# Optimization experiments

Measured on AMD Instinct MI355X. Metric: run time of the kernel, lower is better.

The kernel has to match this reference:

```python
import jax, jax.numpy as jnp
import numpy as np

B, T, HID = 1, 2048, 1024
H, D = 16, 64
S = 64            # selection_block_size / sliding window / compress block
MAXK = 8          # max_selected_blocks
W_ENT, W_SP = 0.01, 0.01
NB = T // S       # 32 blocks (T divisible by S -> no padding branch)


def setup_inputs() -> dict:
    key = jax.random.key(0)
    ks = jax.random.split(key, 8)
    rn = lambda k, shp, s=0.02: jax.random.normal(k, shp, jnp.float32) * s
    return {
        'hidden_states': rn(ks[0], (B, T, HID), 1.0),
        'Wq': rn(ks[1], (HID, H * D)),
        'Wk': rn(ks[2], (HID, H * D)),
        'Wv': rn(ks[3], (HID, H * D)),
        'Wo': rn(ks[4], (H * D, HID)),
        'Wc': rn(ks[5], (S * D, D)),      # shared k/v compress MLP (same module in torch)
        'bc': jnp.zeros((D,), jnp.float32),
        'k_scale': jnp.ones((1,), jnp.float32),
        'k_bias': jnp.zeros((1,), jnp.float32),
        'Ws': rn(ks[6], (HID, 3 * H)),
        'bs': jnp.zeros((3 * H,), jnp.float32),
    }


def _local_attn(q, k, v):
    # lucidrains LocalAttention: window S, causal, look_backward=1, scale d^-0.5
    b, h, t, d = q.shape
    nw = t // S
    qw = q.reshape(b, h, nw, S, d)
    kw = k.reshape(b, h, nw, S, d)
    vw = v.reshape(b, h, nw, S, d)
    k_prev = jnp.concatenate([jnp.zeros_like(kw[:, :, :1]), kw[:, :, :-1]], axis=2)
    v_prev = jnp.concatenate([jnp.zeros_like(vw[:, :, :1]), vw[:, :, :-1]], axis=2)
    kc = jnp.concatenate([k_prev, kw], axis=3)   # (b,h,nw,2S,d)
    vc = jnp.concatenate([v_prev, vw], axis=3)
    scores = jnp.einsum('bhwid,bhwjd->bhwij', qw, kc) / jnp.sqrt(jnp.float32(d))
    qpos = jnp.arange(S)[:, None]
    krel = jnp.arange(2 * S)[None, :] - S        # key pos relative to window start
    wins = jnp.arange(nw)[:, None, None]
    allowed = (krel <= qpos)[None] & (wins * S + krel[None] >= 0)  # (nw,S,2S)
    NEG = -jnp.finfo(scores.dtype).max
    scores = jnp.where(allowed[None, None], scores, NEG)
    p = jax.nn.softmax(scores, axis=-1)
    return jnp.einsum('bhwij,bhwjd->bhwid', p, vc).reshape(b, h, t, d)


def reference(hidden_states, Wq, Wk, Wv, Wo, Wc, bc, k_scale, k_bias, Ws, bs):
    x = hidden_states
    scale = 1.0 / jnp.sqrt(jnp.float32(D))
    q = (x @ Wq).reshape(B, T, H, D).transpose(0, 2, 1, 3)
    k = (x @ Wk).reshape(B, T, H, D).transpose(0, 2, 1, 3)
    v = (x @ Wv).reshape(B, T, H, D).transpose(0, 2, 1, 3)

    sliding_out = _local_attn(q, k, v)

    # block compression (shared MLP for k and v, exact-erf GELU as in torch)
    k_blk = k.reshape(B, H, NB, S * D)
    v_blk = v.reshape(B, H, NB, S * D)
    kc = jax.nn.gelu(k_blk @ Wc + bc, approximate=False)   # (B,H,NB,D)
    vc = jax.nn.gelu(v_blk @ Wc + bc, approximate=False)

    importance = jnp.einsum('bhid,bhjd->bhij', q, kc) * scale   # (B,H,T,NB)
    comp_probs = jax.nn.softmax(importance, axis=-1)
    comp_out = jnp.einsum('bhij,bhjd->bhid', comp_probs, vc)

    # per-query-block scores, entropy-driven dynamic k
    block_scores = importance.reshape(B, H, NB, S, NB).mean(axis=3)   # (B,H,NB,NB)
    block_probs = jax.nn.softmax(block_scores, axis=-1)
    entropy = -jnp.sum(block_probs * jnp.log(block_probs + 1e-9), axis=-1)
    max_entropy = jnp.log(jnp.float32(NB))
    norm_ent = entropy / (max_entropy + 1e-9)
    k_ratio = jax.nn.sigmoid(k_scale[0] * norm_ent + k_bias[0])
    dynamic_k = jnp.clip(MAXK * k_ratio, 1.0, float(MAXK)).astype(jnp.int32)  # torch .long() truncates
    avg_k = dynamic_k.astype(jnp.float32).mean()

    _, topk_idx = jax.lax.top_k(block_scores, MAXK)                 # (B,H,NB,MAXK)
    k_mask = jnp.arange(MAXK)[None, None, None, :] < dynamic_k[..., None]
    sel = (topk_idx[..., None] == jnp.arange(NB)) & k_mask[..., None]
    mask = sel.any(axis=-2)                                         # (B,H,NB,NB)
    mask = mask | jnp.eye(NB, dtype=bool)[None, None]
    sparse_mask = jnp.repeat(jnp.repeat(mask, S, axis=2), S, axis=3)  # (B,H,T,T)

    attn = jnp.einsum('bhid,bhjd->bhij', q, k) * scale
    NEG = -jnp.finfo(attn.dtype).max
    attn = jnp.where(sparse_mask, attn, NEG)
    fine_probs = jax.nn.softmax(attn, axis=-1)
    fine_out = jnp.einsum('bhij,bhjd->bhid', fine_probs, v)

    strategy = jax.nn.sigmoid(x @ Ws + bs).reshape(B, T, H, 3).transpose(0, 2, 1, 3)  # (B,H,T,3)
    combined = jnp.stack([sliding_out, comp_out, fine_out], axis=-1)  # (B,H,T,D,3)
    out = jnp.einsum('bhnds,bhns->bhnd', combined, strategy)
    merged = out.transpose(0, 2, 1, 3).reshape(B, T, H * D)
    output = merged @ Wo

    entropy_loss = jnp.mean((k_ratio - norm_ent) ** 2)
    aux_loss = W_ENT * entropy_loss + W_SP * k_ratio.mean()
    return output, avg_k, aux_loss
```

## Files before the change

### kernel.cpp

```cpp
#include <hip/hip_runtime.h>
#include <math.h>
#include <stdint.h>

typedef unsigned short u16;
typedef short v8s __attribute__((ext_vector_type(8)));
typedef float v4f __attribute__((ext_vector_type(4)));

constexpr int kT   = 2048;
constexpr int kHID = 1024;
constexpr int kH   = 16;
constexpr int kNB  = 32;
constexpr size_t MB = 1ull << 20;

__device__ __forceinline__ float b2f(u16 u) { unsigned x = ((unsigned)u) << 16; return __uint_as_float(x); }
__device__ __forceinline__ u16 f2b(float f) {
  unsigned x = __float_as_uint(f);
  x += 0x7FFFu + ((x >> 16) & 1u);
  return (u16)(x >> 16);
}
__device__ __forceinline__ v4f mfma16(v8s a, v8s b, v4f c) {
  return __builtin_amdgcn_mfma_f32_16x16x32_bf16(a, b, c, 0, 0, 0);
}
__device__ __forceinline__ void gl_lds16(const void* g, void* l) {
  __builtin_amdgcn_global_load_lds((const __attribute__((address_space(1))) uint32_t*)g,
                                   (__attribute__((address_space(3))) uint32_t*)l, 16, 0, 0);
}

__global__ __launch_bounds__(256) void prep_kernel(
    const float* __restrict__ x, const float* __restrict__ Wq, const float* __restrict__ Wk,
    const float* __restrict__ Wv, const float* __restrict__ Wo, const float* __restrict__ Wc,
    const float* __restrict__ Wsp,
    u16* __restrict__ xh,
    u16* __restrict__ WqtH, u16* __restrict__ WktH,
    u16* __restrict__ WvtH, u16* __restrict__ WotH, u16* __restrict__ WctH, u16* __restrict__ WctL,
    u16* __restrict__ Wst) {
  __shared__ float tbuf[32][33];
  int bid = blockIdx.x;
  const int tid = threadIdx.x;
  if (bid < 1024) {
    int i = bid * 2048 + tid * 8;
    float4 a = *(const float4*)(x + i), b = *(const float4*)(x + i + 4);
    float tv[8] = {a.x, a.y, a.z, a.w, b.x, b.y, b.z, b.w};
    union { u16 s[8]; uint4 u; } hs;
#pragma unroll
    for (int e = 0; e < 8; ++e) hs.s[e] = f2b(tv[e]);
    *(uint4*)(xh + i) = hs.u;
    return;
  }
  bid -= 1024;
  const float* W; u16* Hh; u16* Ll; int Kd, Nd, bx, by;
  if (bid < 4096) {
    int wsel = bid >> 10, sub = bid & 1023;
    W  = wsel == 0 ? Wq : wsel == 1 ? Wk : wsel == 2 ? Wv : Wo;
    Hh = wsel == 0 ? WqtH : wsel == 1 ? WktH : wsel == 2 ? WvtH : WotH;
    Ll = nullptr;
    Kd = 1024; Nd = 1024;
    bx = (sub & 31) * 32; by = (sub >> 5) * 32;
  } else if (bid < 4096 + 256) {
    int sub = bid - 4096;
    W = Wc; Hh = WctH; Ll = WctL;
    Kd = 4096; Nd = 64;
    bx = (sub & 1) * 32; by = (sub >> 1) * 32;
  } else {
    int i = (bid - 4096 - 256) * 256 + tid;
    int n = i >> 10, k2 = i & 1023;
    float v = (n < 48) ? Wsp[(size_t)k2 * 48 + n] : 0.f;
    Wst[(size_t)n * 1024 + k2] = f2b(v);
    return;
  }
  const int lx = tid & 31, ly = tid >> 5;
  for (int i2 = ly; i2 < 32; i2 += 8) tbuf[i2][lx] = W[(size_t)(by + i2) * Nd + bx + lx];
  __syncthreads();
  for (int i2 = ly; i2 < 32; i2 += 8) {
    float xv = tbuf[lx][i2];
    size_t idx = (size_t)(bx + i2) * Kd + by + lx;
    u16 h = f2b(xv);
    Hh[idx] = h;
    if (Ll) Ll[idx] = f2b(xv - b2f(h));
  }
}

__global__ __launch_bounds__(256) void proj_gemm(const u16* __restrict__ xh,
                                                 const u16* __restrict__ WkH, const u16* __restrict__ WqH,
                                                 const u16* __restrict__ WvH, const u16* __restrict__ Wst,
                                                 const float* __restrict__ bsp,
                                                 u16* __restrict__ kbf, u16* __restrict__ qh,
                                                 u16* __restrict__ vbf, float* __restrict__ strat) {
  __shared__ u16 AsH[128 * 64], BsH[128 * 64];
  const int b = blockIdx.x;
  const int g = (b & 7) * 50 + (b >> 3);
  const int role = g >> 4, bmi = g & 15;
  int z, bni;
  if (role < 8)       { z = 0; bni = role; }
  else if (role < 16) { z = 1; bni = role - 8; }
  else if (role < 24) { z = 2; bni = role - 16; }
  else                { z = 3; bni = 0; }
  const int bm = bmi * 128, bn = bni * 128;
  const u16* Bh = (z == 0) ? WkH : (z == 1) ? WqH : (z == 2) ? WvH : Wst;
  const int tid = threadIdx.x, w = tid >> 6, lane = tid & 63;
  const int lg = lane >> 4, l16 = lane & 15;
  const int wr = w >> 1, wc = w & 1;
  v4f acc[4][4] = {};
  for (int k0 = 0; k0 < kHID; k0 += 64) {
    __syncthreads();
#pragma unroll
    for (int p = 0; p < 4; ++p) {
      int s = tid + p * 256, row = s >> 3, sf = (s & 7) ^ (row & 7);
      gl_lds16(xh + (size_t)(bm + row) * kHID + k0 + sf * 8, (char*)AsH + s * 16);
      gl_lds16(Bh + (size_t)(bn + row) * kHID + k0 + sf * 8, (char*)BsH + s * 16);
    }
    __syncthreads();
#pragma unroll
    for (int kk = 0; kk < 2; ++kk) {
      v8s bh4[4];
#pragma unroll
      for (int j = 0; j < 4; ++j) {
        int col = wc * 64 + j * 16 + l16;
        bh4[j] = *(const v8s*)((const char*)BsH + col * 128 + (((kk * 4 + lg) ^ (col & 7)) * 16));
      }
#pragma unroll
      for (int i = 0; i < 4; ++i) {
        int row = wr * 64 + i * 16 + l16;
        v8s ah = *(const v8s*)((const char*)AsH + row * 128 + (((kk * 4 + lg) ^ (row & 7)) * 16));
#pragma unroll
        for (int j = 0; j < 4; ++j) acc[i][j] = mfma16(ah, bh4[j], acc[i][j]);
      }
    }
  }
#pragma unroll
  for (int i = 0; i < 4; ++i)
#pragma unroll
    for (int j = 0; j < 4; ++j)
#pragma unroll
      for (int r = 0; r < 4; ++r) {
        int row = bm + wr * 64 + i * 16 + lg * 4 + r;
        int col = bn + wc * 64 + j * 16 + l16;
        float val = acc[i][j][r];
        if (z == 3) {
          if (col < 48) strat[(size_t)row * 48 + col] = 1.f / (1.f + expf(-(val + bsp[col])));
        } else {
          u16 hh = f2b(val);
          size_t idx = (size_t)row * kHID + col;
          if (z == 0) kbf[idx] = hh;
          else if (z == 1) qh[idx] = hh;
          else vbf[idx] = hh;
        }
      }
}

__global__ __launch_bounds__(256) void cgemm_fused(const u16* __restrict__ kbf,
                                                   const u16* __restrict__ vbf,
                                                   const u16* __restrict__ WcH, const u16* __restrict__ WcL,
                                                   float* __restrict__ Pk, float* __restrict__ Pv) {
  __shared__ u16 AsH[64 * 64], BsH[64 * 64], BsL[64 * 64];
  const int bm = blockIdx.y * 64;
  const int isK = (blockIdx.z < 8);
  const int ks = isK ? blockIdx.z : blockIdx.z - 8;
  const u16* Asrc = isK ? kbf : vbf;
  float* P = isK ? Pk : Pv;
  const int tid = threadIdx.x;
  const int w = tid >> 6, lane = tid & 63;
  const int lg = lane >> 4, l16 = lane & 15;
  const int wr = w >> 1, wc = w & 1;
  v4f acc[2][2] = {};
  for (int k0 = ks * 512; k0 < ks * 512 + 512; k0 += 64) {
    __syncthreads();
#pragma unroll
    for (int ss = 0; ss < 2; ++ss) {
      int s = tid + ss * 256, row = s >> 3, sf = (s & 7) ^ (row & 7);
      int r = bm + row;
      size_t abase = ((size_t)((r & 31) * 64 + (k0 >> 6))) * kHID + (r >> 5) * 64 + sf * 8;
      gl_lds16(Asrc + abase, (char*)AsH + s * 16);
      gl_lds16(WcH + (size_t)row * 4096 + k0 + sf * 8, (char*)BsH + s * 16);
      if (isK) gl_lds16(WcL + (size_t)row * 4096 + k0 + sf * 8, (char*)BsL + s * 16);
    }
    __syncthreads();
    v8s ah[2][2], bh[2][2];
#pragma unroll
    for (int i = 0; i < 2; ++i)
#pragma unroll
      for (int kk = 0; kk < 2; ++kk) {
        int row = wr * 32 + i * 16 + l16;
        ah[i][kk] = *(const v8s*)((const char*)AsH + row * 128 + (((kk * 4 + lg) ^ (row & 7)) * 16));
        int col = wc * 32 + i * 16 + l16;
        bh[i][kk] = *(const v8s*)((const char*)BsH + col * 128 + (((kk * 4 + lg) ^ (col & 7)) * 16));
      }
#pragma unroll
    for (int i = 0; i < 2; ++i)
#pragma unroll
      for (int j = 0; j < 2; ++j) {
        acc[i][j] = mfma16(ah[i][0], bh[j][0], acc[i][j]);
        acc[i][j] = mfma16(ah[i][1], bh[j][1], acc[i][j]);
      }
    if (isK) {
      v8s bl[2][2];
#pragma unroll
      for (int i = 0; i < 2; ++i)
#pragma unroll
        for (int kk = 0; kk < 2; ++kk) {
          int col = wc * 32 + i * 16 + l16;
          bl[i][kk] = *(const v8s*)((const char*)BsL + col * 128 + (((kk * 4 + lg) ^ (col & 7)) * 16));
        }
#pragma unroll
      for (int i = 0; i < 2; ++i)
#pragma unroll
        for (int j = 0; j < 2; ++j) {
          acc[i][j] = mfma16(ah[i][0], bl[j][0], acc[i][j]);
          acc[i][j] = mfma16(ah[i][1], bl[j][1], acc[i][j]);
        }
    }
  }
#pragma unroll
  for (int i = 0; i < 2; ++i)
#pragma unroll
    for (int j = 0; j < 2; ++j)
#pragma unroll
      for (int r = 0; r < 4; ++r) {
        int row = bm + wr * 32 + i * 16 + lg * 4 + r;
        int col = wc * 32 + j * 16 + l16;
        P[(size_t)ks * 32768 + (size_t)row * 64 + col] = acc[i][j][r];
      }
}

__global__ __launch_bounds__(256) void creduce_kernel(const float* __restrict__ Pk,
                                                      const float* __restrict__ Pv,
                                                      const float* __restrict__ bc,
                                                      u16* __restrict__ kch, u16* __restrict__ kcl,
                                                      u16* __restrict__ vct) {
  int idx = blockIdx.x * 256 + threadIdx.x;
  int which = idx >> 15;
  int e = idx & 32767;
  const float* P = which ? Pv : Pk;
  float s = 0.f;
#pragma unroll
  for (int ks = 0; ks < 8; ++ks) s += P[(size_t)ks * 32768 + e];
  s += bc[e & 63];
  float g = 0.5f * s * (1.f + erff(s * 0.70710678118654752f));
  if (!which) {
    u16 hh = f2b(g);
    kch[e] = hh;
    kcl[e] = f2b(g - b2f(hh));
  } else {
    int h2 = e >> 11, j = (e >> 6) & 31, d = e & 63;
    vct[(size_t)h2 * 2048 + d * 32 + j] = f2b(g);
  }
}

__global__ __launch_bounds__(256) void impsel_mfma(const u16* __restrict__ qh,
                                                   const u16* __restrict__ kch,
                                                   const u16* __restrict__ kcl,
                                                   const u16* __restrict__ vct,
                                                   const float* __restrict__ strat,
                                                   const float* __restrict__ kscale_p,
                                                   const float* __restrict__ kbias_p,
                                                   unsigned* __restrict__ maskb,
                                                   float* __restrict__ krb,
                                                   float* __restrict__ neb,
                                                   int* __restrict__ dkb,
                                                   u16* __restrict__ merged) {
  __shared__ u16 Pl[4][16 * 32];
  __shared__ float red[4][32];
  const int tt = blockIdx.x, h = blockIdx.y;
  const int tid = threadIdx.x, w = tid >> 6, lane = tid & 63;
  const int lg = lane >> 4, l16 = lane & 15;
  const size_t qoff = (size_t)(tt * 64 + w * 16 + l16) * kHID + h * 64;
  v8s ah[2];
  ah[0] = *(const v8s*)(qh + qoff + lg * 8);
  ah[1] = *(const v8s*)(qh + qoff + 32 + lg * 8);
  v4f sa[2] = {};
#pragma unroll
  for (int ct = 0; ct < 2; ++ct) {
    int col = ct * 16 + l16;
#pragma unroll
    for (int kk = 0; kk < 2; ++kk) {
      v8s bh = *(const v8s*)(kch + ((size_t)h * 32 + col) * 64 + kk * 32 + lg * 8);
      v8s bl = *(const v8s*)(kcl + ((size_t)h * 32 + col) * 64 + kk * 32 + lg * 8);
      sa[ct] = mfma16(ah[kk], bh, sa[ct]);
      sa[ct] = mfma16(ah[kk], bl, sa[ct]);
    }
  }
#pragma unroll
  for (int ct = 0; ct < 2; ++ct)
#pragma unroll
    for (int j = 0; j < 4; ++j) sa[ct][j] *= 0.125f;
#pragma unroll
  for (int ct = 0; ct < 2; ++ct) {
    float v = sa[ct][0] + sa[ct][1] + sa[ct][2] + sa[ct][3];
    v += __shfl_xor(v, 16, 64);
    v += __shfl_xor(v, 32, 64);
    if (lg == 0) red[w][ct * 16 + l16] = v;
  }
  float linv[4];
#pragma unroll
  for (int j = 0; j < 4; ++j) {
    float m = fmaxf(sa[0][j], sa[1][j]);
#pragma unroll
    for (int mm = 1; mm < 16; mm <<= 1) m = fmaxf(m, __shfl_xor(m, mm, 64));
    float e0 = __expf(sa[0][j] - m), e1 = __expf(sa[1][j] - m);
    float s = e0 + e1;
#pragma unroll
    for (int mm = 1; mm < 16; mm <<= 1) s += __shfl_xor(s, mm, 64);
    linv[j] = 1.f / s;
    int row = lg * 4 + j;
    Pl[w][row * 32 + l16] = f2b(e0);
    Pl[w][row * 32 + 16 + l16] = f2b(e1);
  }
  v8s pa = *(const v8s*)(&Pl[w][l16 * 32 + lg * 8]);
  v4f o[4] = {};
#pragma unroll
  for (int dt = 0; dt < 4; ++dt) {
    v8s b = *(const v8s*)(vct + ((size_t)h * 64 + dt * 16 + l16) * 32 + lg * 8);
    o[dt] = mfma16(pa, b, o[dt]);
  }
#pragma unroll
  for (int dt = 0; dt < 4; ++dt)
#pragma unroll
    for (int j = 0; j < 4; ++j) {
      int t = tt * 64 + w * 16 + lg * 4 + j;
      int d = dt * 16 + l16;
      size_t mi = (size_t)t * kHID + h * 64 + d;
      merged[mi] = f2b(strat[t * 48 + h * 3 + 1] * (o[dt][j] * linv[j]));
    }
  __syncthreads();
  if (w == 0) {
    const int j = lane & 31;
    float bsj = (red[0][j] + red[1][j] + red[2][j] + red[3][j]) * (1.f / 64.f);
    float mx = bsj;
#pragma unroll
    for (int m = 1; m < 32; m <<= 1) mx = fmaxf(mx, __shfl_xor(mx, m, 64));
    float e = expf(bsj - mx);
    float lsum = e;
#pragma unroll
    for (int m = 1; m < 32; m <<= 1) lsum += __shfl_xor(lsum, m, 64);
    float p = e / lsum;
    float ent = p * logf(p + 1e-9f);
#pragma unroll
    for (int m = 1; m < 32; m <<= 1) ent += __shfl_xor(ent, m, 64);
    ent = -ent;
    float ne = ent / (logf(32.f) + 1e-9f);
    float kr = 1.f / (1.f + expf(-(kscale_p[0] * ne + kbias_p[0])));
    int dk = (int)fminf(fmaxf(8.f * kr, 1.f), 8.f);
    unsigned mword = 1u << tt;
    int taken = 0;
    for (int r = 0; r < dk; ++r) {
      float v2 = taken ? -3.4e38f : bsj;
      int idx2 = j;
#pragma unroll
      for (int m = 1; m < 32; m <<= 1) {
        float ov = __shfl_xor(v2, m, 64);
        int oi = __shfl_xor(idx2, m, 64);
        if (ov > v2 || (ov == v2 && oi < idx2)) { v2 = ov; idx2 = oi; }
      }
      mword |= (1u << idx2);
      if (j == idx2) taken = 1;
    }
    if (lane == 0) {
      maskb[h * kNB + tt] = mword;
      krb[h * kNB + tt] = kr;
      neb[h * kNB + tt] = ne;
      dkb[h * kNB + tt] = dk;
    }
  }
}

__global__ void finalize_kernel(const int* __restrict__ dkb, const float* __restrict__ krb,
                                const float* __restrict__ neb, float* __restrict__ out) {
  __shared__ float s1[512], s2[512], s3[512];
  int t2 = threadIdx.x;
  float fdk = (float)dkb[t2], kr = krb[t2], ne = neb[t2];
  float d = kr - ne;
  s1[t2] = fdk; s2[t2] = d * d; s3[t2] = kr;
  __syncthreads();
  for (int st = 256; st > 0; st >>= 1) {
    if (t2 < st) { s1[t2] += s1[t2 + st]; s2[t2] += s2[t2 + st]; s3[t2] += s3[t2 + st]; }
    __syncthreads();
  }
  if (t2 == 0) {
    out[(size_t)kT * kHID + 0] = s1[0] * (1.f / 512.f);
    out[(size_t)kT * kHID + 1] = 0.01f * (s2[0] * (1.f / 512.f)) + 0.01f * (s3[0] * (1.f / 512.f));
  }
}

__global__ __launch_bounds__(256) void fineslide_mfma(const u16* __restrict__ qh,
                                                      const u16* __restrict__ kb_,
                                                      const u16* __restrict__ vb_,
                                                      const float* __restrict__ strat,
                                                      const unsigned* __restrict__ maskb,
                                                      u16* __restrict__ merged) {
  __shared__ u16 Kb[64 * 64];
  __shared__ u16 Vt[64 * 64];
  __shared__ u16 Pl[4][16 * 64];
  const int b = blockIdx.x;
  const int xcd = b & 7, slot = b >> 3;
  const int h = xcd + 8 * (slot >> 5);
  const int qb = slot & 31;
  const unsigned mword = maskb[h * kNB + qb];
  unsigned uni = mword | (1u << qb);
  if (qb > 0) uni |= 1u << (qb - 1);
  const int tid = threadIdx.x, w = tid >> 6, lane = tid & 63;
  const int lg = lane >> 4, l16 = lane & 15;
  v8s aq[2];
  {
    const u16* qrow = qh + (size_t)(qb * 64 + w * 16 + l16) * kHID + h * 64;
    aq[0] = *(const v8s*)(qrow + lg * 8);
    aq[1] = *(const v8s*)(qrow + 32 + lg * 8);
  }
  float mF[4], lF[4], mS[4], lS[4];
  v4f oF[4] = {}, oS[4] = {};
#pragma unroll
  for (int j = 0; j < 4; ++j) { mF[j] = -1e30f; lF[j] = 0.f; mS[j] = -1e30f; lS[j] = 0.f; }

  auto upd = [&](v4f* sa, float* m_run, float* l_run, v4f* o_acc) {
    float corr[4];
#pragma unroll
    for (int j = 0; j < 4; ++j) {
      float t = fmaxf(fmaxf(sa[0][j], sa[1][j]), fmaxf(sa[2][j], sa[3][j]));
#pragma unroll
      for (int mm = 1; mm < 16; mm <<= 1) t = fmaxf(t, __shfl_xor(t, mm, 64));
      float mn = fmaxf(m_run[j], t);
      corr[j] = __expf(m_run[j] - mn);
      m_run[j] = mn;
    }
    float rs[4] = {0.f, 0.f, 0.f, 0.f};
    float pv[4][4];
#pragma unroll
    for (int ct = 0; ct < 4; ++ct)
#pragma unroll
      for (int j = 0; j < 4; ++j) {
        float e = __expf(sa[ct][j] - m_run[j]);
        pv[ct][j] = e;
        rs[j] += e;
      }
#pragma unroll
    for (int j = 0; j < 4; ++j) {
#pragma unroll
      for (int mm = 1; mm < 16; mm <<= 1) rs[j] += __shfl_xor(rs[j], mm, 64);
      l_run[j] = l_run[j] * corr[j] + rs[j];
    }
#pragma unroll
    for (int ct = 0; ct < 4; ++ct)
#pragma unroll
      for (int j = 0; j < 4; ++j) {
        int row = lg * 4 + j;
        int seg = ct * 2 + (l16 >> 3);
        *((u16*)((char*)Pl + w * 2048 + row * 128 + ((seg ^ (row & 7)) * 16)) + (l16 & 7)) = f2b(pv[ct][j]);
      }
#pragma unroll
    for (int dt = 0; dt < 4; ++dt)
#pragma unroll
      for (int j = 0; j < 4; ++j) o_acc[dt][j] *= corr[j];
#pragma unroll
    for (int dt = 0; dt < 4; ++dt) {
      int d = dt * 16 + l16;
#pragma unroll
      for (int kk = 0; kk < 2; ++kk) {
        v8s pa = *(const v8s*)((const char*)Pl + w * 2048 + l16 * 128 + (((kk * 4 + lg) ^ (l16 & 7)) * 16));
        v8s vb2 = *(const v8s*)((const char*)Vt + d * 128 + (((kk * 4 + lg) ^ (d & 7)) * 16));
        o_acc[dt] = mfma16(pa, vb2, o_acc[dt]);
      }
    }
  };

  for (int jb = 0; jb < 32; ++jb) {
    if (!((uni >> jb) & 1u)) continue;
    __syncthreads();
#pragma unroll
    for (int ss = 0; ss < 2; ++ss) {
      int s = tid + ss * 256;
      int key = s >> 3, sf = (s & 7) ^ (key & 7);
      gl_lds16(kb_ + (size_t)(jb * 64 + key) * kHID + h * 64 + sf * 8, (char*)Kb + s * 16);
    }
    {
      int key = tid & 63, d0 = (tid >> 6) * 16;
      const u16* vsrc = vb_ + (size_t)(jb * 64 + key) * kHID + h * 64 + d0;
      union { uint4 u[2]; u16 s[16]; } c;
      c.u[0] = *(const uint4*)(vsrc);
      c.u[1] = *(const uint4*)(vsrc + 8);
#pragma unroll
      for (int i = 0; i < 16; ++i) {
        int d = d0 + i;
        *((u16*)((char*)Vt + d * 128 + (((key >> 3) ^ (d & 7)) * 16)) + (key & 7)) = c.s[i];
      }
    }
    __syncthreads();
    v4f sa[4] = {};
#pragma unroll
    for (int ct = 0; ct < 4; ++ct) {
      int key = ct * 16 + l16;
#pragma unroll
      for (int kk = 0; kk < 2; ++kk) {
        v8s bk = *(const v8s*)((const char*)Kb + key * 128 + (((kk * 4 + lg) ^ (key & 7)) * 16));
        sa[ct] = mfma16(aq[kk], bk, sa[ct]);
      }
    }
#pragma unroll
    for (int ct = 0; ct < 4; ++ct)
#pragma unroll
      for (int j = 0; j < 4; ++j) sa[ct][j] *= 0.125f;
    const bool inF = (mword >> jb) & 1u;
    const bool inS = (jb == qb) || (jb + 1 == qb);
    if (inF) upd(sa, mF, lF, oF);
    if (inS) {
      v4f sb[4];
#pragma unroll
      for (int ct = 0; ct < 4; ++ct) sb[ct] = sa[ct];
      if (jb == qb) {
#pragma unroll
        for (int ct = 0; ct < 4; ++ct) {
          int key = ct * 16 + l16;
#pragma unroll
          for (int j = 0; j < 4; ++j) {
            int qp = w * 16 + lg * 4 + j;
            if (key > qp) sb[ct][j] = -1e30f;
          }
        }
      }
      upd(sb, mS, lS, oS);
    }
  }
#pragma unroll
  for (int dt = 0; dt < 4; ++dt)
#pragma unroll
    for (int j = 0; j < 4; ++j) {
      int row = lg * 4 + j;
      int t = qb * 64 + w * 16 + row;
      int d = dt * 16 + l16;
      size_t idx = (size_t)t * kHID + h * 64 + d;
      float add = strat[t * 48 + h * 3 + 0] * (oS[dt][j] / lS[j]) +
                  strat[t * 48 + h * 3 + 2] * (oF[dt][j] / lF[j]);
      merged[idx] = f2b(b2f(merged[idx]) + add);
    }
}

__global__ __launch_bounds__(256) void gemm_out(const u16* __restrict__ A, const u16* __restrict__ Bt,
                                                float* __restrict__ Cf) {
  __shared__ u16 As[128 * 64], Bs[64 * 64];
  const int b = blockIdx.x;
  const int g = (b & 7) * 32 + (b >> 3);
  const int bn = (g >> 4) * 64;
  const int bm = (g & 15) * 128;
  const int tid = threadIdx.x, w = tid >> 6, lane = tid & 63;
  const int lg = lane >> 4, l16 = lane & 15;
  const int K = kHID;
  v4f acc[2][4] = {};
  for (int k0 = 0; k0 < K; k0 += 64) {
    __syncthreads();
#pragma unroll
    for (int p = 0; p < 4; ++p) {
      int s = tid + p * 256, row = s >> 3, sf = (s & 7) ^ (row & 7);
      gl_lds16(A + (size_t)(bm + row) * K + k0 + sf * 8, (char*)As + s * 16);
    }
#pragma unroll
    for (int p = 0; p < 2; ++p) {
      int s = tid + p * 256, row = s >> 3, sf = (s & 7) ^ (row & 7);
      gl_lds16(Bt + (size_t)(bn + row) * K + k0 + sf * 8, (char*)Bs + s * 16);
    }
    __syncthreads();
    v8s a[2][2], bfr[4][2];
#pragma unroll
    for (int i = 0; i < 2; ++i)
#pragma unroll
      for (int kk = 0; kk < 2; ++kk) {
        int row = w * 32 + i * 16 + l16;
        a[i][kk] = *(const v8s*)((const char*)As + row * 128 + (((kk * 4 + lg) ^ (row & 7)) * 16));
      }
#pragma unroll
    for (int j = 0; j < 4; ++j)
#pragma unroll
      for (int kk = 0; kk < 2; ++kk) {
        int col = j * 16 + l16;
        bfr[j][kk] = *(const v8s*)((const char*)Bs + col * 128 + (((kk * 4 + lg) ^ (col & 7)) * 16));
      }
#pragma unroll
    for (int i = 0; i < 2; ++i)
#pragma unroll
      for (int j = 0; j < 4; ++j) {
        acc[i][j] = mfma16(a[i][0], bfr[j][0], acc[i][j]);
        acc[i][j] = mfma16(a[i][1], bfr[j][1], acc[i][j]);
      }
  }
#pragma unroll
  for (int i = 0; i < 2; ++i)
#pragma unroll
    for (int j = 0; j < 4; ++j)
#pragma unroll
      for (int r = 0; r < 4; ++r) {
        int row = bm + w * 32 + i * 16 + lg * 4 + r;
        int col = bn + j * 16 + l16;
        Cf[(size_t)row * kHID + col] = acc[i][j][r];
      }
}

extern "C" void kernel_launch(void* const* d_in, const int* in_sizes, int n_in,
                              void* d_out, int out_size, void* d_ws, size_t ws_size,
                              hipStream_t stream) {
  const float* x      = (const float*)d_in[0];
  const float* Wq     = (const float*)d_in[1];
  const float* Wk     = (const float*)d_in[2];
  const float* Wv     = (const float*)d_in[3];
  const float* Wo     = (const float*)d_in[4];
  const float* Wc     = (const float*)d_in[5];
  const float* bc     = (const float*)d_in[6];
  const float* kscale = (const float*)d_in[7];
  const float* kbias  = (const float*)d_in[8];
  const float* Wsp    = (const float*)d_in[9];
  const float* bsp    = (const float*)d_in[10];
  float* out = (float*)d_out;
  char* W = (char*)d_ws;

  u16* qh     = (u16*)(W + 0 * MB);
  u16* kbf    = (u16*)(W + 8 * MB);
  u16* vbf    = (u16*)(W + 16 * MB);
  u16* merged = (u16*)(W + 20 * MB);
  u16* xh     = (u16*)(W + 24 * MB);
  u16* WqtH   = (u16*)(W + 32 * MB);
  u16* WktH   = (u16*)(W + 36 * MB);
  u16* WvtH   = (u16*)(W + 40 * MB);
  u16* WotH   = (u16*)(W + 42 * MB);
  u16* WctH   = (u16*)(W + 44 * MB);
  u16* WctL   = (u16*)(W + 44 * MB + 512 * 1024);
  u16* Wst    = (u16*)(W + 45 * MB);
  float* strat= (float*)(W + 46 * MB);
  float* Pk   = (float*)(W + 47 * MB);
  float* Pv   = (float*)(W + 48 * MB);
  u16* kchb   = (u16*)(W + 49 * MB);
  u16* kclb   = (u16*)(W + 49 * MB + 64 * 1024);
  u16* vctb   = (u16*)(W + 49 * MB + 128 * 1024);
  unsigned* maskb = (unsigned*)(W + 49 * MB + 192 * 1024);
  float* krb  = (float*)(W + 49 * MB + 196 * 1024);
  float* neb  = (float*)(W + 49 * MB + 200 * 1024);
  int*   dkb  = (int*)(W + 49 * MB + 204 * 1024);

  dim3 b256(256);
  prep_kernel<<<5888, b256, 0, stream>>>(x, Wq, Wk, Wv, Wo, Wc, Wsp,
                                         xh, WqtH, WktH, WvtH, WotH, WctH, WctL, Wst);
  proj_gemm<<<400, b256, 0, stream>>>(xh, WktH, WqtH, WvtH, Wst,
                                      bsp, kbf, qh, vbf, strat);
  cgemm_fused<<<dim3(1, 8, 16), b256, 0, stream>>>(kbf, vbf, WctH, WctL, Pk, Pv);
  creduce_kernel<<<256, b256, 0, stream>>>(Pk, Pv, bc, kchb, kclb, vctb);
  impsel_mfma<<<dim3(32, kH), b256, 0, stream>>>(qh, kchb, kclb, vctb, strat,
                                                 kscale, kbias, maskb, krb, neb, dkb, merged);
  finalize_kernel<<<1, 512, 0, stream>>>(dkb, krb, neb, out);
  fineslide_mfma<<<512, b256, 0, stream>>>(qh, kbf, vbf, strat, maskb, merged);
  gemm_out<<<256, b256, 0, stream>>>(merged, WotH, out);
}
```

Baseline: 104.4 us.

## Halve proj_gemm M-tile and double-buffer K/V tiles in fineslide attention

The projection GEMM now uses 64-row M tiles, so it launches 800 blocks instead of 400. This spreads the 25 panels across more workgroups and is meant to improve occupancy and fill the GPU. The fineslide attention kernel now double-buffers its K and V LDS tiles and walks the selected blocks by bit iteration. It prefetches the next block's K (async to LDS) and V (into registers) while computing the current one, with one barrier per iteration instead of two. The tradeoffs are more LDS per block, lower reuse of each weight tile in the projection, and more registers.

New measurement: 96.20 us. 7.8% less time.

```diff
diff --git a/kernel.cpp b/kernel.cpp
--- a/kernel.cpp
+++ b/kernel.cpp
@@ -86,27 +86,31 @@
                                                  const float* __restrict__ bsp,
                                                  u16* __restrict__ kbf, u16* __restrict__ qh,
                                                  u16* __restrict__ vbf, float* __restrict__ strat) {
-  __shared__ u16 AsH[128 * 64], BsH[128 * 64];
+  __shared__ u16 AsH[64 * 64], BsH[128 * 64];
   const int b = blockIdx.x;
-  const int g = (b & 7) * 50 + (b >> 3);
-  const int role = g >> 4, bmi = g & 15;
+  const int slot = (b & 7) * 100 + (b >> 3);
+  const int panel = slot >> 5, bmi = slot & 31;
   int z, bni;
-  if (role < 8)       { z = 0; bni = role; }
-  else if (role < 16) { z = 1; bni = role - 8; }
-  else if (role < 24) { z = 2; bni = role - 16; }
-  else                { z = 3; bni = 0; }
-  const int bm = bmi * 128, bn = bni * 128;
+  if (panel < 8)       { z = 0; bni = panel; }
+  else if (panel < 16) { z = 1; bni = panel - 8; }
+  else if (panel < 24) { z = 2; bni = panel - 16; }
+  else                 { z = 3; bni = 0; }
+  const int bm = bmi * 64, bn = bni * 128;
   const u16* Bh = (z == 0) ? WkH : (z == 1) ? WqH : (z == 2) ? WvH : Wst;
   const int tid = threadIdx.x, w = tid >> 6, lane = tid & 63;
   const int lg = lane >> 4, l16 = lane & 15;
   const int wr = w >> 1, wc = w & 1;
-  v4f acc[4][4] = {};
+  v4f acc[2][4] = {};
   for (int k0 = 0; k0 < kHID; k0 += 64) {
     __syncthreads();
+#pragma unroll
+    for (int p = 0; p < 2; ++p) {
+      int s = tid + p * 256, row = s >> 3, sf = (s & 7) ^ (row & 7);
+      gl_lds16(xh + (size_t)(bm + row) * kHID + k0 + sf * 8, (char*)AsH + s * 16);
+    }
 #pragma unroll
     for (int p = 0; p < 4; ++p) {
       int s = tid + p * 256, row = s >> 3, sf = (s & 7) ^ (row & 7);
-      gl_lds16(xh + (size_t)(bm + row) * kHID + k0 + sf * 8, (char*)AsH + s * 16);
       gl_lds16(Bh + (size_t)(bn + row) * kHID + k0 + sf * 8, (char*)BsH + s * 16);
     }
     __syncthreads();
@@ -119,8 +123,8 @@
         bh4[j] = *(const v8s*)((const char*)BsH + col * 128 + (((kk * 4 + lg) ^ (col & 7)) * 16));
       }
 #pragma unroll
-      for (int i = 0; i < 4; ++i) {
-        int row = wr * 64 + i * 16 + l16;
+      for (int i = 0; i < 2; ++i) {
+        int row = wr * 32 + i * 16 + l16;
         v8s ah = *(const v8s*)((const char*)AsH + row * 128 + (((kk * 4 + lg) ^ (row & 7)) * 16));
 #pragma unroll
         for (int j = 0; j < 4; ++j) acc[i][j] = mfma16(ah, bh4[j], acc[i][j]);
@@ -128,12 +132,12 @@
     }
   }
 #pragma unroll
-  for (int i = 0; i < 4; ++i)
+  for (int i = 0; i < 2; ++i)
 #pragma unroll
     for (int j = 0; j < 4; ++j)
 #pragma unroll
       for (int r = 0; r < 4; ++r) {
-        int row = bm + wr * 64 + i * 16 + lg * 4 + r;
+        int row = bm + wr * 32 + i * 16 + lg * 4 + r;
         int col = bn + wc * 64 + j * 16 + l16;
         float val = acc[i][j][r];
         if (z == 3) {
@@ -387,8 +391,8 @@
                                                       const float* __restrict__ strat,
                                                       const unsigned* __restrict__ maskb,
                                                       u16* __restrict__ merged) {
-  __shared__ u16 Kb[64 * 64];
-  __shared__ u16 Vt[64 * 64];
+  __shared__ u16 Kb[2][64 * 64];
+  __shared__ u16 Vt[2][64 * 64];
   __shared__ u16 Pl[4][16 * 64];
   const int b = blockIdx.x;
   const int xcd = b & 7, slot = b >> 3;
@@ -410,7 +414,32 @@
 #pragma unroll
   for (int j = 0; j < 4; ++j) { mF[j] = -1e30f; lF[j] = 0.f; mS[j] = -1e30f; lS[j] = 0.f; }
 
-  auto upd = [&](v4f* sa, float* m_run, float* l_run, v4f* o_acc) {
+  const int vkey = tid & 63, vd0 = (tid >> 6) * 16;
+
+  auto k_stage = [&](int buf, int jb) {
+#pragma unroll
+    for (int ss = 0; ss < 2; ++ss) {
+      int s = tid + ss * 256;
+      int key = s >> 3, sf = (s & 7) ^ (key & 7);
+      gl_lds16(kb_ + (size_t)(jb * 64 + key) * kHID + h * 64 + sf * 8, (char*)Kb[buf] + s * 16);
+    }
+  };
+  auto v_issue = [&](int jb, uint4& c0, uint4& c1) {
+    const u16* vsrc = vb_ + (size_t)(jb * 64 + vkey) * kHID + h * 64 + vd0;
+    c0 = *(const uint4*)(vsrc);
+    c1 = *(const uint4*)(vsrc + 8);
+  };
+  auto v_write = [&](int buf, uint4 c0, uint4 c1) {
+    union { uint4 u[2]; u16 s[16]; } c;
+    c.u[0] = c0; c.u[1] = c1;
+#pragma unroll
+    for (int i = 0; i < 16; ++i) {
+      int d = vd0 + i;
+      *((u16*)((char*)Vt[buf] + d * 128 + (((vkey >> 3) ^ (d & 7)) * 16)) + (vkey & 7)) = c.s[i];
+    }
+  };
+
+  auto upd = [&](const v4f* sa, float* m_run, float* l_run, v4f* o_acc, int buf) {
     float corr[4];
 #pragma unroll
     for (int j = 0; j < 4; ++j) {
@@ -455,41 +484,31 @@
 #pragma unroll
       for (int kk = 0; kk < 2; ++kk) {
         v8s pa = *(const v8s*)((const char*)Pl + w * 2048 + l16 * 128 + (((kk * 4 + lg) ^ (l16 & 7)) * 16));
-        v8s vb2 = *(const v8s*)((const char*)Vt + d * 128 + (((kk * 4 + lg) ^ (d & 7)) * 16));
+        v8s vb2 = *(const v8s*)((const char*)Vt[buf] + d * 128 + (((kk * 4 + lg) ^ (d & 7)) * 16));
         o_acc[dt] = mfma16(pa, vb2, o_acc[dt]);
       }
     }
   };
 
-  for (int jb = 0; jb < 32; ++jb) {
-    if (!((uni >> jb) & 1u)) continue;
-    __syncthreads();
-#pragma unroll
-    for (int ss = 0; ss < 2; ++ss) {
-      int s = tid + ss * 256;
-      int key = s >> 3, sf = (s & 7) ^ (key & 7);
-      gl_lds16(kb_ + (size_t)(jb * 64 + key) * kHID + h * 64 + sf * 8, (char*)Kb + s * 16);
-    }
-    {
-      int key = tid & 63, d0 = (tid >> 6) * 16;
-      const u16* vsrc = vb_ + (size_t)(jb * 64 + key) * kHID + h * 64 + d0;
-      union { uint4 u[2]; u16 s[16]; } c;
-      c.u[0] = *(const uint4*)(vsrc);
-      c.u[1] = *(const uint4*)(vsrc + 8);
-#pragma unroll
-      for (int i = 0; i < 16; ++i) {
-        int d = d0 + i;
-        *((u16*)((char*)Vt + d * 128 + (((key >> 3) ^ (d & 7)) * 16)) + (key & 7)) = c.s[i];
-      }
-    }
-    __syncthreads();
+  int jb_cur = __builtin_ctz(uni);
+  unsigned rem = uni & (uni - 1);
+  uint4 vc0, vc1;
+  v_issue(jb_cur, vc0, vc1);
+  k_stage(0, jb_cur);
+  v_write(0, vc0, vc1);
+  int buf = 0;
+  while (jb_cur >= 0) {
+    int jb_next = -1;
+    if (rem) { jb_next = __builtin_ctz(rem); rem &= rem - 1; }
+    __syncthreads();
+    if (jb_next >= 0) { v_issue(jb_next, vc0, vc1); k_stage(buf ^ 1, jb_next); }
     v4f sa[4] = {};
 #pragma unroll
     for (int ct = 0; ct < 4; ++ct) {
       int key = ct * 16 + l16;
 #pragma unroll
       for (int kk = 0; kk < 2; ++kk) {
-        v8s bk = *(const v8s*)((const char*)Kb + key * 128 + (((kk * 4 + lg) ^ (key & 7)) * 16));
+        v8s bk = *(const v8s*)((const char*)Kb[buf] + key * 128 + (((kk * 4 + lg) ^ (key & 7)) * 16));
         sa[ct] = mfma16(aq[kk], bk, sa[ct]);
       }
     }
@@ -497,14 +516,14 @@
     for (int ct = 0; ct < 4; ++ct)
 #pragma unroll
       for (int j = 0; j < 4; ++j) sa[ct][j] *= 0.125f;
-    const bool inF = (mword >> jb) & 1u;
-    const bool inS = (jb == qb) || (jb + 1 == qb);
-    if (inF) upd(sa, mF, lF, oF);
+    const bool inF = (mword >> jb_cur) & 1u;
+    const bool inS = (jb_cur == qb) || (jb_cur + 1 == qb);
+    if (inF) upd(sa, mF, lF, oF, buf);
     if (inS) {
       v4f sb[4];
 #pragma unroll
       for (int ct = 0; ct < 4; ++ct) sb[ct] = sa[ct];
-      if (jb == qb) {
+      if (jb_cur == qb) {
 #pragma unroll
         for (int ct = 0; ct < 4; ++ct) {
           int key = ct * 16 + l16;
@@ -515,8 +534,11 @@
           }
         }
       }
-      upd(sb, mS, lS, oS);
-    }
+      upd(sb, mS, lS, oS, buf);
+    }
+    if (jb_next >= 0) v_write(buf ^ 1, vc0, vc1);
+    jb_cur = jb_next;
+    buf ^= 1;
   }
 #pragma unroll
   for (int dt = 0; dt < 4; ++dt)
@@ -634,7 +656,7 @@
   dim3 b256(256);
   prep_kernel<<<5888, b256, 0, stream>>>(x, Wq, Wk, Wv, Wo, Wc, Wsp,
                                          xh, WqtH, WktH, WvtH, WotH, WctH, WctL, Wst);
-  proj_gemm<<<400, b256, 0, stream>>>(xh, WktH, WqtH, WvtH, Wst,
+  proj_gemm<<<800, b256, 0, stream>>>(xh, WktH, WqtH, WvtH, Wst,
                                       bsp, kbf, qh, vbf, strat);
   cgemm_fused<<<dim3(1, 8, 16), b256, 0, stream>>>(kbf, vbf, WctH, WctL, Pk, Pv);
   creduce_kernel<<<256, b256, 0, stream>>>(Pk, Pv, bc, kchb, kclb, vctb);
```
